# Optimization experiments

Hardware: AMD Instinct MI355X
Metric: run time of the kernel (lower is better)

The kernel has to match this reference:

```python
import jax, jax.numpy as jnp
import numpy as np
import math

B, S, D, H = 2, 2048, 1024, 16
DK = D // H
SCALE = math.sqrt(DK)
NEG_BIG = -1e9


def setup_inputs() -> dict:
    key = jax.random.key(0)
    ks = jax.random.split(key, 7)
    x = jax.random.normal(ks[0], (B, S, D), dtype=jnp.float32)
    # additive causal mask: 0 on/below diagonal, -inf above
    causal = jnp.triu(jnp.ones((S, S), dtype=bool), k=1)
    mask = jnp.where(causal, -jnp.inf, 0.0).astype(jnp.float32)
    key_padding_mask = jax.random.bernoulli(ks[1], 0.1, (B, S))
    init = 1.0 / math.sqrt(D)
    Wq = jax.random.normal(ks[2], (D, D), dtype=jnp.float32) * init
    Wk = jax.random.normal(ks[3], (D, D), dtype=jnp.float32) * init
    Wv = jax.random.normal(ks[4], (D, D), dtype=jnp.float32) * init
    Wo = jax.random.normal(ks[5], (D, D), dtype=jnp.float32) * init
    bo = jnp.zeros((D,), dtype=jnp.float32)
    return {"x": x, "mask": mask, "key_padding_mask": key_padding_mask,
            "Wq": Wq, "Wk": Wk, "Wv": Wv, "Wo": Wo, "bo": bo}


def reference(x, mask, key_padding_mask, Wq, Wk, Wv, Wo, bo):
    b, s, d = x.shape
    # project and split heads -> [B,H,S,Dk]
    def heads(W):
        return jnp.einsum('bsd,de->bse', x, W).reshape(b, s, H, DK).transpose(0, 2, 1, 3)
    Q, K, V = heads(Wq), heads(Wk), heads(Wv)
    scores = jnp.einsum('bhqd,bhkd->bhqk', Q, K) / SCALE          # [B,H,S,S]
    scores = scores + mask[None, None]                            # additive attn mask
    scores = jnp.where(key_padding_mask[:, None, None, :], -jnp.inf, scores)
    # rows whose max is -inf (fully masked) get all scores set to -1e9
    max_scores = jnp.max(scores, axis=-1, keepdims=True)
    scores = jnp.where(jnp.isinf(max_scores), NEG_BIG, scores)
    attn = jax.nn.softmax(scores, axis=-1)
    attn = jnp.where(jnp.isnan(attn), 0.0, attn)
    # dropout is identity in eval mode
    ctx = jnp.einsum('bhqk,bhkd->bhqd', attn, V)                  # [B,H,S,Dk]
    ctx = ctx.transpose(0, 2, 1, 3).reshape(b, s, d)
    return jnp.einsum('bsd,de->bse', ctx, Wo) + bo
```

## Files before the change

### kernel.cpp

```cpp
#include <hip/hip_runtime.h>
#include <stdint.h>

#define NB 2
#define NS 2048
#define ND 1024
#define NH 16
#define NDK 64

typedef __attribute__((ext_vector_type(8))) short s8v;
typedef __attribute__((ext_vector_type(4))) float f4v;
typedef __attribute__((ext_vector_type(4))) unsigned short us4v;
typedef __attribute__((ext_vector_type(8))) unsigned short us8v;
typedef __attribute__((ext_vector_type(2))) uint32_t u2v;

__device__ __forceinline__ unsigned short f2bf(float f) {
  uint32_t u = __builtin_bit_cast(uint32_t, f);
  u = (u + 0x7fffu + ((u >> 16) & 1u)) >> 16;
  return (unsigned short)u;
}
__device__ __forceinline__ float bf2f(unsigned short h) {
  uint32_t u = ((uint32_t)h) << 16;
  return __builtin_bit_cast(float, u);
}
__device__ __forceinline__ uint32_t cvtpk(float lo, float hi) {
  uint32_t r;
  asm("v_cvt_pk_bf16_f32 %0, %1, %2" : "=v"(r) : "v"(lo), "v"(hi));
  return r;
}

__device__ __forceinline__ void gload16(const void* g, void* l) {
  __builtin_amdgcn_global_load_lds(
      (const __attribute__((address_space(1))) void*)g,
      (__attribute__((address_space(3))) void*)l, 16, 0, 0);
}

__global__ void k_convert_x(const float* __restrict__ x, unsigned short* __restrict__ xbf) {
  int i = (blockIdx.x * 256 + threadIdx.x) * 4;
  float4 v = *(const float4*)(x + i);
  us4v o;
  o[0] = f2bf(v.x); o[1] = f2bf(v.y); o[2] = f2bf(v.z); o[3] = f2bf(v.w);
  *(us4v*)(xbf + i) = o;
}

__global__ void k_transpose_w(const float* __restrict__ Wq, const float* __restrict__ Wk,
                              const float* __restrict__ Wv, const float* __restrict__ Wo,
                              unsigned short* __restrict__ wt_qkv, unsigned short* __restrict__ wt_o) {
  __shared__ float tls[64][65];
  int bid = blockIdx.x;
  int mat = bid >> 8;
  int tile = bid & 255;
  int tk = tile >> 4, tn = tile & 15;
  const float* W = (mat == 0) ? Wq : (mat == 1) ? Wk : (mat == 2) ? Wv : Wo;
  int t = threadIdx.x;
  int lr = t >> 2;
  int lc0 = (t & 3) * 16;
  const float* src = W + (size_t)(tk * 64 + lr) * 1024 + tn * 64 + lc0;
#pragma unroll
  for (int j = 0; j < 16; j += 4) {
    float4 v = *(const float4*)(src + j);
    tls[lr][lc0 + j + 0] = v.x; tls[lr][lc0 + j + 1] = v.y;
    tls[lr][lc0 + j + 2] = v.z; tls[lr][lc0 + j + 3] = v.w;
  }
  __syncthreads();
  float scale = (mat == 0) ? 0.18033688f : 1.0f;
  int nr = t >> 2, kc0 = (t & 3) * 16;
  unsigned short* dst = ((mat < 3) ? (wt_qkv + (size_t)(mat * 1024 + tn * 64 + nr) * 1024)
                                   : (wt_o + (size_t)(tn * 64 + nr) * 1024)) + tk * 64 + kc0;
  us8v o0, o1;
#pragma unroll
  for (int j = 0; j < 8; j++) o0[j] = f2bf(tls[kc0 + j][nr] * scale);
#pragma unroll
  for (int j = 0; j < 8; j++) o1[j] = f2bf(tls[kc0 + 8 + j][nr] * scale);
  *(us8v*)(dst) = o0;
  *(us8v*)(dst + 8) = o1;
}

template <int MODE>
__global__ __launch_bounds__(256) void k_gemm(const unsigned short* __restrict__ A,
                                              const unsigned short* __restrict__ Bt,
                                              unsigned short* __restrict__ qklin,
                                              unsigned short* __restrict__ vt,
                                              const float* __restrict__ bias,
                                              float* __restrict__ out) {
  __shared__ unsigned short lds_a[2][128 * 64];
  __shared__ unsigned short lds_b[2][128 * 64];
  const int K = 1024;
  const int NT = K / 64;
  int bid = blockIdx.x;
  int xcd = bid & 7, local = bid >> 3;
  int m0 = (xcd * 4 + (local & 3)) * 128;
  int n0 = (local >> 2) * 128;
  int tid = threadIdx.x, lane = tid & 63, w = tid >> 6;
  int wm = w >> 1, wn = w & 1;
  int g = lane >> 4, c0 = lane & 15;
  int rrel = lane >> 3;
  int gran = lane & 7;
  f4v acc[4][4];
#pragma unroll
  for (int mi = 0; mi < 4; mi++)
#pragma unroll
    for (int ni = 0; ni < 4; ni++) acc[mi][ni] = (f4v){0.f, 0.f, 0.f, 0.f};

#define STAGE(kt_, buf_)                                                        \
  do {                                                                          \
    int koff = (kt_)*64;                                                        \
    _Pragma("unroll") for (int i = 0; i < 4; i++) {                             \
      int r = 32 * w + 8 * i + rrel;                                            \
      gload16(A + (size_t)(m0 + r) * K + koff + 8 * (gran ^ rrel),              \
              (void*)(lds_a[buf_] + (32 * w + 8 * i) * 64));                    \
      gload16(Bt + (size_t)(n0 + r) * K + koff + 8 * (gran ^ rrel),             \
              (void*)(lds_b[buf_] + (32 * w + 8 * i) * 64));                    \
    }                                                                           \
  } while (0)

  STAGE(0, 0);
  __syncthreads();

  for (int kt = 0; kt < NT; ++kt) {
    int cur = kt & 1;
    if (kt + 1 < NT) STAGE(kt + 1, cur ^ 1);
#pragma unroll
    for (int c = 0; c < 2; c++) {
      s8v af[4], bfr[4];
#pragma unroll
      for (int mi = 0; mi < 4; mi++) {
        int row = 64 * wm + 16 * mi + c0;
        af[mi] = *(const s8v*)(lds_a[cur] + row * 64 + 8 * ((g + 4 * c) ^ (c0 & 7)));
      }
#pragma unroll
      for (int ni = 0; ni < 4; ni++) {
        int row = 64 * wn + 16 * ni + c0;
        bfr[ni] = *(const s8v*)(lds_b[cur] + row * 64 + 8 * ((g + 4 * c) ^ (c0 & 7)));
      }
#pragma unroll
      for (int mi = 0; mi < 4; mi++)
#pragma unroll
        for (int ni = 0; ni < 4; ni++)
          acc[mi][ni] = __builtin_amdgcn_mfma_f32_16x16x32_bf16(af[mi], bfr[ni], acc[mi][ni], 0, 0, 0);
    }
    __syncthreads();
  }
#undef STAGE

#pragma unroll
  for (int mi = 0; mi < 4; mi++)
#pragma unroll
    for (int ni = 0; ni < 4; ni++)
#pragma unroll
      for (int r = 0; r < 4; r++) {
        int m = m0 + 64 * wm + 16 * mi + 4 * g + r;
        int n = n0 + 64 * wn + 16 * ni + c0;
        float v = acc[mi][ni][r];
        if (MODE == 0) {
          unsigned short hv = f2bf(v);
          if (n < 2048) {
            qklin[(size_t)m * 2048 + n] = hv;
          } else {
            int b = m >> 11, s = m & 2047;
            int hh = (n - 2048) >> 6, dk = n & 63;
            vt[(size_t)((b * 16 + hh) * 64 + dk) * 2048 + s] = hv;
          }
        } else {
          out[(size_t)m * 1024 + n] = v + bias[n];
        }
      }
}

__global__ void k_vmean(const unsigned short* __restrict__ vt, float* __restrict__ vmean) {
  int row = blockIdx.x * 4 + (threadIdx.x >> 6);
  int lane = threadIdx.x & 63;
  const unsigned short* p = vt + (size_t)row * 2048 + lane * 32;
  float s = 0.f;
#pragma unroll
  for (int j = 0; j < 32; j += 8) {
    us8v v = *(const us8v*)(p + j);
#pragma unroll
    for (int e = 0; e < 8; e++) s += bf2f(v[e]);
  }
#pragma unroll
  for (int m = 1; m < 64; m <<= 1) s += __shfl_xor(s, m);
  if (lane == 0) vmean[row] = s * (1.0f / 2048.0f);
}

__global__ __launch_bounds__(256) void k_attn(const unsigned short* __restrict__ qklin,
                                              const unsigned short* __restrict__ vt,
                                              const int* __restrict__ kpm,
                                              const float* __restrict__ vmean,
                                              unsigned short* __restrict__ ctx) {
  __shared__ unsigned short lds_k[2][64 * 64];
  __shared__ unsigned short lds_v[2][64 * 64];
  __shared__ unsigned short p_lds[4][16 * 64];
  int wg = blockIdx.x;
  int w5 = wg >> 5, bh = wg & 31;
  int qt = (w5 < 8) ? 31 - w5 : (w5 < 16) ? w5 - 8 : (w5 < 24) ? 39 - w5 : w5 - 16;
  int b = bh >> 4, h = bh & 15;
  int tid = threadIdx.x, lane = tid & 63, w = tid >> 6;
  int g = lane >> 4, c0 = lane & 15;
  int q0 = qt * 64 + w * 16;
  unsigned short* pl = p_lds[w];
  int rrel = lane >> 3, gran = lane & 7;

  const unsigned short* ksrc0 = qklin + (size_t)(b * NS) * 2048 + 1024 + h * 64;
  const unsigned short* vsrc0 = vt + (size_t)(bh * 64) * 2048;

  const unsigned short* qbase = qklin + (size_t)(b * NS + q0 + c0) * 2048 + h * 64 + 8 * g;
  s8v qf0 = *(const s8v*)(qbase);
  s8v qf1 = *(const s8v*)(qbase + 32);

  f4v cacc[4];
#pragma unroll
  for (int d = 0; d < 4; d++) cacc[d] = (f4v){0.f, 0.f, 0.f, 0.f};
  float m_s = -1e30f, l_s = 0.f;
  int qrow = q0 + c0;

#define STAGEKV(it_, buf_)                                                      \
  do {                                                                          \
    int kb_ = (it_)*64;                                                         \
    _Pragma("unroll") for (int i = 0; i < 2; i++) {                             \
      int r = 16 * w + 8 * i + rrel;                                            \
      gload16(ksrc0 + (size_t)(kb_ + r) * 2048 + 8 * (gran ^ rrel),             \
              (void*)(lds_k[buf_] + (16 * w + 8 * i) * 64));                    \
      gload16(vsrc0 + (size_t)r * 2048 + kb_ + 8 * (gran ^ rrel),               \
              (void*)(lds_v[buf_] + (16 * w + 8 * i) * 64));                    \
    }                                                                           \
  } while (0)

  STAGEKV(0, 0);
  int kp_cur = kpm[b * NS + lane];

  int nkt = qt + 1;
  for (int it = 0; it < nkt; ++it) {
    int kb = it * 64;
    int cur = it & 1;
    int kp_next = 0;
    if (it + 1 < nkt) {
      STAGEKV(it + 1, cur ^ 1);
      kp_next = kpm[b * NS + (it + 1) * 64 + lane];
      asm volatile("s_waitcnt vmcnt(5)" ::: "memory");
    } else {
      asm volatile("s_waitcnt vmcnt(0)" ::: "memory");
    }
    __builtin_amdgcn_s_barrier();
    __builtin_amdgcn_sched_barrier(0);
    uint64_t padmask = __ballot(kp_cur != 0);
    f4v sacc[4];
#pragma unroll
    for (int t = 0; t < 4; t++) {
      int row = 16 * t + c0;
      s8v kf0 = *(const s8v*)(lds_k[cur] + row * 64 + 8 * (g ^ (c0 & 7)));
      s8v kf1 = *(const s8v*)(lds_k[cur] + row * 64 + 8 * ((4 + g) ^ (c0 & 7)));
      f4v z = (f4v){0.f, 0.f, 0.f, 0.f};
      z = __builtin_amdgcn_mfma_f32_16x16x32_bf16(kf0, qf0, z, 0, 0, 0);
      z = __builtin_amdgcn_mfma_f32_16x16x32_bf16(kf1, qf1, z, 0, 0, 0);
      sacc[t] = z;
    }
    int thr = qrow - kb;
    uint64_t cmask = (thr >= 63) ? ~0ull : ((2ull << thr) - 1ull);
    uint64_t valid = cmask & ~padmask;
    uint32_t vlo = (uint32_t)valid, vhi = (uint32_t)(valid >> 32);
    float p[4][4];
    float mx = -1e30f;
#pragma unroll
    for (int t = 0; t < 4; t++) {
      uint32_t half = (t & 2) ? vhi : vlo;
      uint32_t nib = (half >> (16 * (t & 1) + 4 * g)) & 0xFu;
#pragma unroll
      for (int r = 0; r < 4; r++) {
        float s = sacc[t][r];
        s = ((nib >> r) & 1u) ? s : -1e30f;
        p[t][r] = s;
      }
      mx = fmaxf(mx, fmaxf(fmaxf(p[t][0], p[t][1]), fmaxf(p[t][2], p[t][3])));
    }
    mx = fmaxf(mx, __shfl_xor(mx, 16));
    mx = fmaxf(mx, __shfl_xor(mx, 32));
    if (!__all(mx <= m_s + 11.0f)) {
      float mnew = fmaxf(m_s, mx);
      float a = __builtin_exp2f(m_s - mnew);
      m_s = mnew;
      l_s *= a;
      int ybase = 20 * g;
#pragma unroll
      for (int r = 0; r < 4; r++) {
        float ar = __shfl(a, ybase + r);
#pragma unroll
        for (int d = 0; d < 4; d++) cacc[d][r] *= ar;
      }
    }
    float rs = 0.f;
#pragma unroll
    for (int t = 0; t < 4; t++)
#pragma unroll
      for (int r = 0; r < 4; r++) {
        float e = __builtin_exp2f(p[t][r] - m_s);
        p[t][r] = e;
        rs += e;
      }
    rs += __shfl_xor(rs, 16);
    rs += __shfl_xor(rs, 32);
    rs = (m_s > -1e29f) ? rs : 0.f;
    l_s += rs;
#pragma unroll
    for (int t = 0; t < 4; t++) {
      u2v pk;
      pk[0] = cvtpk(p[t][0], p[t][1]);
      pk[1] = cvtpk(p[t][2], p[t][3]);
      int gr = (2 * t + (g >> 1)) ^ (c0 & 7);
      *(u2v*)((char*)pl + c0 * 128 + gr * 16 + 8 * (g & 1)) = pk;
    }
    asm volatile("s_waitcnt lgkmcnt(0)" ::: "memory");
    __builtin_amdgcn_sched_barrier(0);
#pragma unroll
    for (int c = 0; c < 2; c++) {
      int off = c0 * 128 + 16 * g + 64 * c;
      off ^= (c0 & 7) << 4;
      s8v pf = *(const s8v*)((const char*)pl + off);
#pragma unroll
      for (int d = 0; d < 4; d++) {
        int row = 16 * d + c0;
        s8v vf = *(const s8v*)(lds_v[cur] + row * 64 + 8 * ((4 * c + g) ^ (c0 & 7)));
        cacc[d] = __builtin_amdgcn_mfma_f32_16x16x32_bf16(pf, vf, cacc[d], 0, 0, 0);
      }
    }
    __builtin_amdgcn_s_barrier();
    __builtin_amdgcn_sched_barrier(0);
    kp_cur = kp_next;
  }
#undef STAGEKV
  float lq[4];
  {
    int ybase = 20 * g;
#pragma unroll
    for (int r = 0; r < 4; r++) lq[r] = __shfl(l_s, ybase + r);
  }
#pragma unroll
  for (int d = 0; d < 4; d++)
#pragma unroll
    for (int r = 0; r < 4; r++) {
      int q = q0 + 4 * g + r;
      float l = lq[r];
      float v = (l > 0.f) ? cacc[d][r] / l : vmean[bh * 64 + 16 * d + c0];
      ctx[(size_t)(b * NS + q) * ND + h * 64 + 16 * d + c0] = f2bf(v);
    }
}

extern "C" void kernel_launch(void* const* d_in, const int* in_sizes, int n_in,
                              void* d_out, int out_size, void* d_ws, size_t ws_size,
                              hipStream_t stream) {
  const float* x  = (const float*)d_in[0];
  const int* kpm  = (const int*)d_in[2];
  const float* Wq = (const float*)d_in[3];
  const float* Wk = (const float*)d_in[4];
  const float* Wv = (const float*)d_in[5];
  const float* Wo = (const float*)d_in[6];
  const float* bo = (const float*)d_in[7];

  char* ws = (char*)d_ws;
  unsigned short* xbf   = (unsigned short*)(ws);
  unsigned short* wtqkv = (unsigned short*)(ws + 8u * 1024 * 1024);
  unsigned short* wto   = (unsigned short*)(ws + 14u * 1024 * 1024);
  unsigned short* vt    = (unsigned short*)(ws + 16u * 1024 * 1024);
  float* vmean          = (float*)(ws + 24u * 1024 * 1024);
  unsigned short* ctx   = xbf;
  unsigned short* qklin = (unsigned short*)d_out;

  k_convert_x<<<4096, 256, 0, stream>>>(x, xbf);
  k_transpose_w<<<1024, 256, 0, stream>>>(Wq, Wk, Wv, Wo, wtqkv, wto);
  k_gemm<0><<<768, 256, 0, stream>>>(xbf, wtqkv, qklin, vt, nullptr, nullptr);
  k_vmean<<<512, 256, 0, stream>>>(vt, vmean);
  k_attn<<<1024, 256, 0, stream>>>(qklin, vt, kpm, vmean, ctx);
  k_gemm<1><<<256, 256, 0, stream>>>(ctx, wto, nullptr, nullptr, bo, (float*)d_out);
}
```

Measured before the change: 142.4 us.

## Enlarge attention query tile to 128 rows, two 16-row blocks per wave

Each workgroup now processes 128 query rows, with each wave handling two 16-row blocks against every staged K/V tile. This halves the number of workgroups and the repeated K/V global loads per query, and reuses each K/V LDS fragment for two MFMA blocks. The costs are more register pressure from doubled accumulators, fewer workgroups (512) for load balance across CUs, and idle waves on diagonal tiles that skip compute but still wait at the barriers.

```diff
diff --git a/kernel.cpp b/kernel.cpp
--- a/kernel.cpp
+++ b/kernel.cpp
@@ -189,29 +189,36 @@
                                               unsigned short* __restrict__ ctx) {
   __shared__ unsigned short lds_k[2][64 * 64];
   __shared__ unsigned short lds_v[2][64 * 64];
-  __shared__ unsigned short p_lds[4][16 * 64];
+  __shared__ unsigned short p_lds[4][32 * 64];
   int wg = blockIdx.x;
-  int w5 = wg >> 5, bh = wg & 31;
-  int qt = (w5 < 8) ? 31 - w5 : (w5 < 16) ? w5 - 8 : (w5 < 24) ? 39 - w5 : w5 - 16;
+  int w4 = wg >> 5, bh = wg & 31;
+  int qt = (w4 < 8) ? 15 - w4 : w4 - 8;
   int b = bh >> 4, h = bh & 15;
   int tid = threadIdx.x, lane = tid & 63, w = tid >> 6;
   int g = lane >> 4, c0 = lane & 15;
-  int q0 = qt * 64 + w * 16;
+  int q0 = qt * 128 + w * 32;
   unsigned short* pl = p_lds[w];
   int rrel = lane >> 3, gran = lane & 7;
 
   const unsigned short* ksrc0 = qklin + (size_t)(b * NS) * 2048 + 1024 + h * 64;
   const unsigned short* vsrc0 = vt + (size_t)(bh * 64) * 2048;
 
-  const unsigned short* qbase = qklin + (size_t)(b * NS + q0 + c0) * 2048 + h * 64 + 8 * g;
-  s8v qf0 = *(const s8v*)(qbase);
-  s8v qf1 = *(const s8v*)(qbase + 32);
-
-  f4v cacc[4];
-#pragma unroll
-  for (int d = 0; d < 4; d++) cacc[d] = (f4v){0.f, 0.f, 0.f, 0.f};
-  float m_s = -1e30f, l_s = 0.f;
-  int qrow = q0 + c0;
+  s8v qf[2][2];
+#pragma unroll
+  for (int blk = 0; blk < 2; blk++) {
+    const unsigned short* qb =
+        qklin + (size_t)(b * NS + q0 + 16 * blk + c0) * 2048 + h * 64 + 8 * g;
+    qf[blk][0] = *(const s8v*)(qb);
+    qf[blk][1] = *(const s8v*)(qb + 32);
+  }
+
+  f4v cacc[2][4];
+#pragma unroll
+  for (int blk = 0; blk < 2; blk++)
+#pragma unroll
+    for (int d = 0; d < 4; d++) cacc[blk][d] = (f4v){0.f, 0.f, 0.f, 0.f};
+  float m_s[2] = {-1e30f, -1e30f}, l_s[2] = {0.f, 0.f};
+  int qrowv[2] = {q0 + c0, q0 + 16 + c0};
 
 #define STAGEKV(it_, buf_)                                                      \
   do {                                                                          \
@@ -228,7 +235,7 @@
   STAGEKV(0, 0);
   int kp_cur = kpm[b * NS + lane];
 
-  int nkt = qt + 1;
+  int nkt = 2 * qt + 2;
   for (int it = 0; it < nkt; ++it) {
     int kb = it * 64;
     int cur = it & 1;
@@ -242,84 +249,113 @@
     }
     __builtin_amdgcn_s_barrier();
     __builtin_amdgcn_sched_barrier(0);
-    uint64_t padmask = __ballot(kp_cur != 0);
-    f4v sacc[4];
-#pragma unroll
-    for (int t = 0; t < 4; t++) {
-      int row = 16 * t + c0;
-      s8v kf0 = *(const s8v*)(lds_k[cur] + row * 64 + 8 * (g ^ (c0 & 7)));
-      s8v kf1 = *(const s8v*)(lds_k[cur] + row * 64 + 8 * ((4 + g) ^ (c0 & 7)));
-      f4v z = (f4v){0.f, 0.f, 0.f, 0.f};
-      z = __builtin_amdgcn_mfma_f32_16x16x32_bf16(kf0, qf0, z, 0, 0, 0);
-      z = __builtin_amdgcn_mfma_f32_16x16x32_bf16(kf1, qf1, z, 0, 0, 0);
-      sacc[t] = z;
-    }
-    int thr = qrow - kb;
-    uint64_t cmask = (thr >= 63) ? ~0ull : ((2ull << thr) - 1ull);
-    uint64_t valid = cmask & ~padmask;
-    uint32_t vlo = (uint32_t)valid, vhi = (uint32_t)(valid >> 32);
-    float p[4][4];
-    float mx = -1e30f;
-#pragma unroll
-    for (int t = 0; t < 4; t++) {
-      uint32_t half = (t & 2) ? vhi : vlo;
-      uint32_t nib = (half >> (16 * (t & 1) + 4 * g)) & 0xFu;
-#pragma unroll
-      for (int r = 0; r < 4; r++) {
-        float s = sacc[t][r];
-        s = ((nib >> r) & 1u) ? s : -1e30f;
-        p[t][r] = s;
-      }
-      mx = fmaxf(mx, fmaxf(fmaxf(p[t][0], p[t][1]), fmaxf(p[t][2], p[t][3])));
-    }
-    mx = fmaxf(mx, __shfl_xor(mx, 16));
-    mx = fmaxf(mx, __shfl_xor(mx, 32));
-    if (!__all(mx <= m_s + 11.0f)) {
-      float mnew = fmaxf(m_s, mx);
-      float a = __builtin_exp2f(m_s - mnew);
-      m_s = mnew;
-      l_s *= a;
-      int ybase = 20 * g;
-#pragma unroll
-      for (int r = 0; r < 4; r++) {
-        float ar = __shfl(a, ybase + r);
-#pragma unroll
-        for (int d = 0; d < 4; d++) cacc[d][r] *= ar;
-      }
-    }
-    float rs = 0.f;
-#pragma unroll
-    for (int t = 0; t < 4; t++)
-#pragma unroll
-      for (int r = 0; r < 4; r++) {
-        float e = __builtin_exp2f(p[t][r] - m_s);
-        p[t][r] = e;
-        rs += e;
-      }
-    rs += __shfl_xor(rs, 16);
-    rs += __shfl_xor(rs, 32);
-    rs = (m_s > -1e29f) ? rs : 0.f;
-    l_s += rs;
-#pragma unroll
-    for (int t = 0; t < 4; t++) {
-      u2v pk;
-      pk[0] = cvtpk(p[t][0], p[t][1]);
-      pk[1] = cvtpk(p[t][2], p[t][3]);
-      int gr = (2 * t + (g >> 1)) ^ (c0 & 7);
-      *(u2v*)((char*)pl + c0 * 128 + gr * 16 + 8 * (g & 1)) = pk;
-    }
-    asm volatile("s_waitcnt lgkmcnt(0)" ::: "memory");
-    __builtin_amdgcn_sched_barrier(0);
-#pragma unroll
-    for (int c = 0; c < 2; c++) {
-      int off = c0 * 128 + 16 * g + 64 * c;
-      off ^= (c0 & 7) << 4;
-      s8v pf = *(const s8v*)((const char*)pl + off);
-#pragma unroll
-      for (int d = 0; d < 4; d++) {
-        int row = 16 * d + c0;
-        s8v vf = *(const s8v*)(lds_v[cur] + row * 64 + 8 * ((4 * c + g) ^ (c0 & 7)));
-        cacc[d] = __builtin_amdgcn_mfma_f32_16x16x32_bf16(pf, vf, cacc[d], 0, 0, 0);
+    if (kb <= q0 + 31) {
+      uint64_t padmask = __ballot(kp_cur != 0);
+      f4v sacc[2][4];
+#pragma unroll
+      for (int t = 0; t < 4; t++) {
+        int row = 16 * t + c0;
+        s8v kf0 = *(const s8v*)(lds_k[cur] + row * 64 + 8 * (g ^ (c0 & 7)));
+        s8v kf1 = *(const s8v*)(lds_k[cur] + row * 64 + 8 * ((4 + g) ^ (c0 & 7)));
+#pragma unroll
+        for (int blk = 0; blk < 2; blk++) {
+          f4v z = (f4v){0.f, 0.f, 0.f, 0.f};
+          z = __builtin_amdgcn_mfma_f32_16x16x32_bf16(kf0, qf[blk][0], z, 0, 0, 0);
+          z = __builtin_amdgcn_mfma_f32_16x16x32_bf16(kf1, qf[blk][1], z, 0, 0, 0);
+          sacc[blk][t] = z;
+        }
+      }
+      float mx[2];
+#pragma unroll
+      for (int blk = 0; blk < 2; blk++) {
+        int thr = qrowv[blk] - kb;
+        int thrc = thr < 0 ? 0 : thr;
+        uint64_t cm = (2ull << thrc) - 1ull;
+        uint64_t cmask = (thr >= 63) ? ~0ull : (thr < 0 ? 0ull : cm);
+        uint64_t valid = cmask & ~padmask;
+        uint32_t vlo = (uint32_t)valid, vhi = (uint32_t)(valid >> 32);
+        float m = -1e30f;
+#pragma unroll
+        for (int t = 0; t < 4; t++) {
+          uint32_t half = (t & 2) ? vhi : vlo;
+          uint32_t nib = (half >> (16 * (t & 1) + 4 * g)) & 0xFu;
+#pragma unroll
+          for (int r = 0; r < 4; r++) {
+            float s = sacc[blk][t][r];
+            s = ((nib >> r) & 1u) ? s : -1e30f;
+            sacc[blk][t][r] = s;
+            m = fmaxf(m, s);
+          }
+        }
+        mx[blk] = m;
+      }
+      mx[0] = fmaxf(mx[0], __shfl_xor(mx[0], 16));
+      mx[0] = fmaxf(mx[0], __shfl_xor(mx[0], 32));
+      mx[1] = fmaxf(mx[1], __shfl_xor(mx[1], 16));
+      mx[1] = fmaxf(mx[1], __shfl_xor(mx[1], 32));
+      bool ok = (mx[0] <= m_s[0] + 11.0f) && (mx[1] <= m_s[1] + 11.0f);
+      if (!__all(ok)) {
+        int ybase = 20 * g;
+#pragma unroll
+        for (int blk = 0; blk < 2; blk++) {
+          float mnew = fmaxf(m_s[blk], mx[blk]);
+          float a = __builtin_exp2f(m_s[blk] - mnew);
+          m_s[blk] = mnew;
+          l_s[blk] *= a;
+#pragma unroll
+          for (int r = 0; r < 4; r++) {
+            float ar = __shfl(a, ybase + r);
+#pragma unroll
+            for (int d = 0; d < 4; d++) cacc[blk][d][r] *= ar;
+          }
+        }
+      }
+#pragma unroll
+      for (int blk = 0; blk < 2; blk++) {
+        float rs = 0.f;
+#pragma unroll
+        for (int t = 0; t < 4; t++)
+#pragma unroll
+          for (int r = 0; r < 4; r++) {
+            float e = __builtin_exp2f(sacc[blk][t][r] - m_s[blk]);
+            sacc[blk][t][r] = e;
+            rs += e;
+          }
+        rs += __shfl_xor(rs, 16);
+        rs += __shfl_xor(rs, 32);
+        rs = (m_s[blk] > -1e29f) ? rs : 0.f;
+        l_s[blk] += rs;
+      }
+#pragma unroll
+      for (int blk = 0; blk < 2; blk++) {
+        int qrl = 16 * blk + c0;
+#pragma unroll
+        for (int t = 0; t < 4; t++) {
+          u2v pk;
+          pk[0] = cvtpk(sacc[blk][t][0], sacc[blk][t][1]);
+          pk[1] = cvtpk(sacc[blk][t][2], sacc[blk][t][3]);
+          int gr = (2 * t + (g >> 1)) ^ (c0 & 7);
+          *(u2v*)((char*)pl + qrl * 128 + gr * 16 + 8 * (g & 1)) = pk;
+        }
+      }
+      asm volatile("s_waitcnt lgkmcnt(0)" ::: "memory");
+      __builtin_amdgcn_sched_barrier(0);
+#pragma unroll
+      for (int c = 0; c < 2; c++) {
+        s8v pf[2];
+#pragma unroll
+        for (int blk = 0; blk < 2; blk++) {
+          int off = (16 * blk + c0) * 128 + 16 * g + 64 * c;
+          off ^= (c0 & 7) << 4;
+          pf[blk] = *(const s8v*)((const char*)pl + off);
+        }
+#pragma unroll
+        for (int d = 0; d < 4; d++) {
+          int row = 16 * d + c0;
+          s8v vf = *(const s8v*)(lds_v[cur] + row * 64 + 8 * ((4 * c + g) ^ (c0 & 7)));
+          cacc[0][d] = __builtin_amdgcn_mfma_f32_16x16x32_bf16(pf[0], vf, cacc[0][d], 0, 0, 0);
+          cacc[1][d] = __builtin_amdgcn_mfma_f32_16x16x32_bf16(pf[1], vf, cacc[1][d], 0, 0, 0);
+        }
       }
     }
     __builtin_amdgcn_s_barrier();
@@ -327,21 +363,22 @@
     kp_cur = kp_next;
   }
 #undef STAGEKV
-  float lq[4];
-  {
-    int ybase = 20 * g;
-#pragma unroll
-    for (int r = 0; r < 4; r++) lq[r] = __shfl(l_s, ybase + r);
-  }
-#pragma unroll
-  for (int d = 0; d < 4; d++)
-#pragma unroll
-    for (int r = 0; r < 4; r++) {
-      int q = q0 + 4 * g + r;
-      float l = lq[r];
-      float v = (l > 0.f) ? cacc[d][r] / l : vmean[bh * 64 + 16 * d + c0];
-      ctx[(size_t)(b * NS + q) * ND + h * 64 + 16 * d + c0] = f2bf(v);
-    }
+  int ybase = 20 * g;
+#pragma unroll
+  for (int blk = 0; blk < 2; blk++) {
+    float lq[4];
+#pragma unroll
+    for (int r = 0; r < 4; r++) lq[r] = __shfl(l_s[blk], ybase + r);
+#pragma unroll
+    for (int d = 0; d < 4; d++)
+#pragma unroll
+      for (int r = 0; r < 4; r++) {
+        int q = q0 + 16 * blk + 4 * g + r;
+        float l = lq[r];
+        float v = (l > 0.f) ? cacc[blk][d][r] / l : vmean[bh * 64 + 16 * d + c0];
+        ctx[(size_t)(b * NS + q) * ND + h * 64 + 16 * d + c0] = f2bf(v);
+      }
+  }
 }
 
 extern "C" void kernel_launch(void* const* d_in, const int* in_sizes, int n_in,
@@ -368,6 +405,6 @@
   k_transpose_w<<<1024, 256, 0, stream>>>(Wq, Wk, Wv, Wo, wtqkv, wto);
   k_gemm<0><<<768, 256, 0, stream>>>(xbf, wtqkv, qklin, vt, nullptr, nullptr);
   k_vmean<<<512, 256, 0, stream>>>(vt, vmean);
-  k_attn<<<1024, 256, 0, stream>>>(qklin, vt, kpm, vmean, ctx);
+  k_attn<<<512, 256, 0, stream>>>(qklin, vt, kpm, vmean, ctx);
   k_gemm<1><<<256, 256, 0, stream>>>(ctx, wto, nullptr, nullptr, bo, (float*)d_out);
 }
```

Measured after the change: 166.6 us. 1.17x slower.
